# Optimization experiments

Hardware: AMD Instinct MI355X
Metric: run time of the kernel (lower is better)

## Reference

```python
import jax, jax.numpy as jnp
import numpy as np
import math

D = 128
LAMBDA_INIT = 0.8 - 0.6 * math.exp(-0.3 * 1)  # depth=1


def _clin(xr, xi, wr, wi, br, bi):
    # complex linear: (xr + i xi) @ (wr + i wi)^T + (br + i bi)
    o_r = jnp.einsum('bhsd,od->bhso', xr, wr) - jnp.einsum('bhsd,od->bhso', xi, wi) + br
    o_i = jnp.einsum('bhsd,od->bhso', xr, wi) + jnp.einsum('bhsd,od->bhso', xi, wr) + bi
    return o_r, o_i


def setup_inputs() -> dict:
    key = jax.random.key(0)
    ks = jax.random.split(key, 32)
    B, H, S = 1, 12, 1024
    shp = (B, H, S, D)
    inp = {}
    names = ['q_r', 'q_i', 'k_r', 'k_i', 'v_r', 'v_i', 'pe_q_r', 'pe_q_i', 'pe_k_r', 'pe_k_i']
    for i, n in enumerate(names):
        inp[n] = jax.random.normal(ks[i], shp, dtype=jnp.float32)
    std = 1.0 / math.sqrt(D)
    inp['qw_r'] = jax.random.normal(ks[10], (2 * D, D), jnp.float32) * std
    inp['qw_i'] = jax.random.normal(ks[11], (2 * D, D), jnp.float32) * std
    inp['qb_r'] = jnp.zeros((2 * D,), jnp.float32)
    inp['qb_i'] = jnp.zeros((2 * D,), jnp.float32)
    for j, p in enumerate(['k', 'v', 'g', 'o']):
        inp[p + 'w_r'] = jax.random.normal(ks[12 + 2 * j], (D, D), jnp.float32) * std
        inp[p + 'w_i'] = jax.random.normal(ks[13 + 2 * j], (D, D), jnp.float32) * std
        inp[p + 'b_r'] = jnp.zeros((D,), jnp.float32)
        inp[p + 'b_i'] = jnp.zeros((D,), jnp.float32)
    inp['lq1'] = jax.random.normal(ks[20], (D,), jnp.float32) * 0.1
    inp['lk1'] = jax.random.normal(ks[21], (D,), jnp.float32) * 0.1
    inp['lq2'] = jax.random.normal(ks[22], (D,), jnp.float32) * 0.1
    inp['lk2'] = jax.random.normal(ks[23], (D,), jnp.float32) * 0.1
    inp['sub_w'] = jnp.ones((2 * D,), jnp.float32)
    return inp


def _forward(q_r, q_i, k_r, k_i, v_r, v_i, pe_q_r, pe_q_i, pe_k_r, pe_k_i,
             qw_r, qw_i, qb_r, qb_i, kw_r, kw_i, kb_r, kb_i,
             vw_r, vw_i, vb_r, vb_i, gw_r, gw_i, gb_r, gb_i,
             ow_r, ow_i, ob_r, ob_i, lq1, lk1, lq2, lk2, sub_w):
    scale = D ** (-0.5)
    qp_r, qp_i = _clin(q_r, q_i, qw_r, qw_i, qb_r, qb_i)   # [B,H,S,2D]
    kp_r, kp_i = _clin(k_r, k_i, kw_r, kw_i, kb_r, kb_i)   # [B,H,S,D]
    vp_r, vp_i = _clin(v_r, v_i, vw_r, vw_i, vb_r, vb_i)
    qp_r = qp_r + jnp.concatenate([pe_q_r, pe_q_r], axis=-1)
    qp_i = qp_i + jnp.concatenate([pe_q_i, pe_q_i], axis=-1)
    kp_r = kp_r + pe_k_r
    kp_i = kp_i + pe_k_i
    q1_r, q2_r = jnp.split(qp_r, 2, axis=-1)
    q1_i, q2_i = jnp.split(qp_i, 2, axis=-1)

    def attn_w(qr, qi):
        s_r = jnp.einsum('bhqd,bhkd->bhqk', qr, kp_r) + jnp.einsum('bhqd,bhkd->bhqk', qi, kp_i)
        s_i = jnp.einsum('bhqd,bhkd->bhqk', qi, kp_r) - jnp.einsum('bhqd,bhkd->bhqk', qr, kp_i)
        mag = jnp.sqrt(s_r ** 2 + s_i ** 2 + 1e-8) * scale
        return jax.nn.softmax(mag.astype(jnp.float32), axis=-1).astype(s_r.dtype)

    w1 = attn_w(q1_r, q1_i)
    w2 = attn_w(q2_r, q2_i)
    a1_r = jnp.einsum('bhqk,bhkd->bhqd', w1, vp_r)
    a1_i = jnp.einsum('bhqk,bhkd->bhqd', w1, vp_i)
    a2_r = jnp.einsum('bhqk,bhkd->bhqd', w2, vp_r)
    a2_i = jnp.einsum('bhqk,bhkd->bhqd', w2, vp_i)
    cat_r = jnp.concatenate([a1_r, a2_r], axis=-1)
    cat_i = jnp.concatenate([a1_i, a2_i], axis=-1)
    rms = jnp.sqrt(jnp.mean(cat_r ** 2 + cat_i ** 2, axis=-1, keepdims=True) + 1e-5)
    cat_r = cat_r / rms * sub_w
    cat_i = cat_i / rms * sub_w
    a1_r, a2_r = jnp.split(cat_r, 2, axis=-1)
    a1_i, a2_i = jnp.split(cat_i, 2, axis=-1)
    lam1 = jnp.exp(jnp.sum(lq1 * lk1))
    lam2 = jnp.exp(jnp.sum(lq2 * lk2))
    lam = jax.nn.sigmoid(lam1 - lam2 + LAMBDA_INIT)
    out_r = a1_r - lam * a2_r
    out_i = a1_i - lam * a2_i
    g_r, g_i = _clin(q_r, q_i, gw_r, gw_i, gb_r, gb_i)
    out_r, out_i = g_r * out_r - g_i * out_i, g_r * out_i + g_i * out_r
    out_r, out_i = _clin(out_r, out_i, ow_r, ow_i, ob_r, ob_i)
    return out_r, out_i


def reference(q_r, q_i, k_r, k_i, v_r, v_i, pe_q_r, pe_q_i, pe_k_r, pe_k_i,
              qw_r, qw_i, qb_r, qb_i, kw_r, kw_i, kb_r, kb_i,
              vw_r, vw_i, vb_r, vb_i, gw_r, gw_i, gb_r, gb_i,
              ow_r, ow_i, ob_r, ob_i, lq1, lk1, lq2, lk2, sub_w):
    return _forward(q_r, q_i, k_r, k_i, v_r, v_i, pe_q_r, pe_q_i, pe_k_r, pe_k_i,
                    qw_r, qw_i, qb_r, qb_i, kw_r, kw_i, kb_r, kb_i,
                    vw_r, vw_i, vb_r, vb_i, gw_r, gw_i, gb_r, gb_i,
                    ow_r, ow_i, ob_r, ob_i, lq1, lk1, lq2, lk2, sub_w)
```

## Files before the change

kernel.cpp:

```cpp
#include <hip/hip_runtime.h>
#include <math.h>

#define H 12
#define S 1024
#define D 128
#define NROWS (H * S)

typedef __attribute__((ext_vector_type(8))) _Float16 f16x8;
typedef __attribute__((ext_vector_type(4))) float f32x4;
typedef __attribute__((ext_vector_type(4))) int i32x4;

__device__ __forceinline__ short f2h(float f) {
    _Float16 h = (_Float16)f;
    return __builtin_bit_cast(short, h);
}
__device__ __forceinline__ f16x8 fneg8(f16x8 v) {
    i32x4 u = __builtin_bit_cast(i32x4, v);
    u ^= (int)0x80008000;
    return __builtin_bit_cast(f16x8, u);
}

#define WS_QP_R   0ULL
#define WS_QP_I   6291456ULL
#define WS_KP_R   12582912ULL
#define WS_KP_I   15728640ULL
#define WS_VPT_R  18874368ULL
#define WS_VPT_I  22020096ULL
#define WS_G_R    25165824ULL
#define WS_G_I    31457280ULL
#define WS_ACAT_R 37748736ULL
#define WS_ACAT_I 50331648ULL
#define WS_LAM    62914560ULL
#define WS_SC     62914816ULL
#define W16_PER_HEAD  4194304ULL

__global__ void lam_kernel(const float* __restrict__ lq1, const float* __restrict__ lk1,
                           const float* __restrict__ lq2, const float* __restrict__ lk2,
                           float* __restrict__ lam_out)
{
    int t = threadIdx.x;
    float p1 = lq1[t] * lk1[t];
    float p2 = lq2[t] * lk2[t];
    #pragma unroll
    for (int off = 32; off; off >>= 1) {
        p1 += __shfl_xor(p1, off);
        p2 += __shfl_xor(p2, off);
    }
    __shared__ float s1[2], s2[2];
    if ((t & 63) == 0) { s1[t >> 6] = p1; s2[t >> 6] = p2; }
    __syncthreads();
    if (t == 0) {
        float l1 = expf(s1[0] + s1[1]);
        float l2 = expf(s2[0] + s2[1]);
        float x = l1 - l2 + 0.3555090675909693f;
        lam_out[0] = 1.0f / (1.0f + expf(-x));
    }
}

__global__ __launch_bounds__(256) void proj_all(
    const float* __restrict__ q_r, const float* __restrict__ q_i,
    const float* __restrict__ k_r, const float* __restrict__ k_i,
    const float* __restrict__ v_r, const float* __restrict__ v_i,
    const float* __restrict__ pe_q_r, const float* __restrict__ pe_q_i,
    const float* __restrict__ pe_k_r, const float* __restrict__ pe_k_i,
    const float* __restrict__ qw_r, const float* __restrict__ qw_i,
    const float* __restrict__ qb_r, const float* __restrict__ qb_i,
    const float* __restrict__ kw_r, const float* __restrict__ kw_i,
    const float* __restrict__ kb_r, const float* __restrict__ kb_i,
    const float* __restrict__ vw_r, const float* __restrict__ vw_i,
    const float* __restrict__ vb_r, const float* __restrict__ vb_i,
    const float* __restrict__ gw_r, const float* __restrict__ gw_i,
    const float* __restrict__ gb_r, const float* __restrict__ gb_i,
    short* __restrict__ qp_r, short* __restrict__ qp_i,
    short* __restrict__ kp_r, short* __restrict__ kp_i,
    short* __restrict__ vpT_r, short* __restrict__ vpT_i,
    float* __restrict__ g_r, float* __restrict__ g_i)
{
    const int y = blockIdx.y;
    const float *xr, *xi, *wr, *wi, *br, *bi, *per = nullptr, *pei = nullptr;
    void *outr_, *outi_;
    int M, omode, col0;
    if (y < 4)      { xr = q_r; xi = q_i; wr = qw_r; wi = qw_i; br = qb_r; bi = qb_i;
                      per = pe_q_r; pei = pe_q_i; outr_ = qp_r; outi_ = qp_i;
                      M = 256; omode = 1; col0 = y * 64; }
    else if (y < 6) { xr = k_r; xi = k_i; wr = kw_r; wi = kw_i; br = kb_r; bi = kb_i;
                      per = pe_k_r; pei = pe_k_i; outr_ = kp_r; outi_ = kp_i;
                      M = 128; omode = 1; col0 = (y - 4) * 64; }
    else if (y < 8) { xr = v_r; xi = v_i; wr = vw_r; wi = vw_i; br = vb_r; bi = vb_i;
                      outr_ = vpT_r; outi_ = vpT_i;
                      M = 128; omode = 2; col0 = (y - 6) * 64; }
    else            { xr = q_r; xi = q_i; wr = gw_r; wi = gw_i; br = gb_r; bi = gb_i;
                      outr_ = g_r; outi_ = g_i;
                      M = 128; omode = 0; col0 = (y - 8) * 64; }

    __shared__ short As[128 * 72], Brs[64 * 72], Bis[64 * 72];
    const int t = threadIdx.x;
    const int row0 = blockIdx.x * 128;
    const int lane = t & 63, wid = t >> 6;
    const int wm = (wid >> 1) * 64, wn = (wid & 1) * 32;
    const int fm = lane & 15, fq = lane >> 4;
    f32x4 zero4 = {0.f, 0.f, 0.f, 0.f};
    f32x4 accr[4][2], acci[4][2];
    #pragma unroll
    for (int i = 0; i < 4; ++i)
        #pragma unroll
        for (int j = 0; j < 2; ++j) { accr[i][j] = zero4; acci[i][j] = zero4; }

    for (int c = 0; c < 4; ++c) {
        const bool hi = (c >= 2);
        const int kb = (c & 1) * 64;
        const float* Asrc = hi ? xi : xr;
        const float* Brsrc = hi ? wi : wr;
        const float* Bisrc = hi ? wr : wi;
        const float bsign = hi ? -1.0f : 1.0f;
        __syncthreads();
        #pragma unroll
        for (int it = 0; it < 8; ++it) {
            int lin = it * 256 + t;
            int r = lin >> 4, k4 = (lin & 15) * 4;
            float4 va = *(const float4*)&Asrc[(size_t)(row0 + r) * 128 + kb + k4];
            *(short4*)&As[r * 72 + k4] = make_short4(f2h(va.x), f2h(va.y), f2h(va.z), f2h(va.w));
        }
        #pragma unroll
        for (int it = 0; it < 4; ++it) {
            int lin = it * 256 + t;
            int r = lin >> 4, k4 = (lin & 15) * 4;
            float4 vr = *(const float4*)&Brsrc[(size_t)(col0 + r) * 128 + kb + k4];
            *(short4*)&Brs[r * 72 + k4] = make_short4(f2h(bsign * vr.x), f2h(bsign * vr.y),
                                                      f2h(bsign * vr.z), f2h(bsign * vr.w));
            float4 vi = *(const float4*)&Bisrc[(size_t)(col0 + r) * 128 + kb + k4];
            *(short4*)&Bis[r * 72 + k4] = make_short4(f2h(vi.x), f2h(vi.y), f2h(vi.z), f2h(vi.w));
        }
        __syncthreads();
        #pragma unroll
        for (int ks = 0; ks < 64; ks += 32) {
            f16x8 bfr[2], bfi[2];
            #pragma unroll
            for (int j = 0; j < 2; ++j) {
                bfr[j] = *(const f16x8*)&Brs[(wn + j * 16 + fm) * 72 + ks + fq * 8];
                bfi[j] = *(const f16x8*)&Bis[(wn + j * 16 + fm) * 72 + ks + fq * 8];
            }
            #pragma unroll
            for (int i = 0; i < 4; ++i) {
                f16x8 a = *(const f16x8*)&As[(wm + i * 16 + fm) * 72 + ks + fq * 8];
                #pragma unroll
                for (int j = 0; j < 2; ++j) {
                    accr[i][j] = __builtin_amdgcn_mfma_f32_16x16x32_f16(a, bfr[j], accr[i][j], 0, 0, 0);
                    acci[i][j] = __builtin_amdgcn_mfma_f32_16x16x32_f16(a, bfi[j], acci[i][j], 0, 0, 0);
                }
            }
        }
    }
    #pragma unroll
    for (int i = 0; i < 4; ++i)
        #pragma unroll
        for (int j = 0; j < 2; ++j) {
            int colc = col0 + wn + j * 16 + fm;
            float bbr = br[colc], bbi = bi[colc];
            if (omode == 2) {
                int rb = row0 + wm + i * 16 + fq * 4;
                int hq = rb >> 10, sq = rb & 1023;
                short4 o_r4 = make_short4(f2h(accr[i][j][0] + bbr), f2h(accr[i][j][1] + bbr),
                                          f2h(accr[i][j][2] + bbr), f2h(accr[i][j][3] + bbr));
                short4 o_i4 = make_short4(f2h(acci[i][j][0] + bbi), f2h(acci[i][j][1] + bbi),
                                          f2h(acci[i][j][2] + bbi), f2h(acci[i][j][3] + bbi));
                size_t ob = ((size_t)(hq * 128 + colc)) * 1024 + sq;
                *(short4*)&((short*)outr_)[ob] = o_r4;
                *(short4*)&((short*)outi_)[ob] = o_i4;
            } else {
                #pragma unroll
                for (int reg = 0; reg < 4; ++reg) {
                    int rr = row0 + wm + i * 16 + fq * 4 + reg;
                    float o_r = accr[i][j][reg] + bbr;
                    float o_i = acci[i][j][reg] + bbi;
                    if (per) {
                        o_r += per[(size_t)rr * 128 + (colc & 127)];
                        o_i += pei[(size_t)rr * 128 + (colc & 127)];
                    }
                    if (omode == 1) {
                        ((short*)outr_)[(size_t)rr * M + colc] = f2h(o_r);
                        ((short*)outi_)[(size_t)rr * M + colc] = f2h(o_i);
                    } else {
                        ((float*)outr_)[(size_t)rr * M + colc] = o_r;
                        ((float*)outi_)[(size_t)rr * M + colc] = o_i;
                    }
                }
            }
        }
}

__global__ __launch_bounds__(256) void oproj_mfma(
    const float* __restrict__ xr, const float* __restrict__ xi,
    const float* __restrict__ wr, const float* __restrict__ wi,
    const float* __restrict__ br, const float* __restrict__ bi,
    float* __restrict__ outr, float* __restrict__ outi)
{
    __shared__ short As[128 * 72], Brs[64 * 72], Bis[64 * 72];
    const int t = threadIdx.x;
    const int row0 = blockIdx.x * 128, col0 = blockIdx.y * 64;
    const int lane = t & 63, wid = t >> 6;
    const int wm = (wid >> 1) * 64, wn = (wid & 1) * 32;
    const int fm = lane & 15, fq = lane >> 4;
    f32x4 zero4 = {0.f, 0.f, 0.f, 0.f};
    f32x4 accr[4][2], acci[4][2];
    #pragma unroll
    for (int i = 0; i < 4; ++i)
        #pragma unroll
        for (int j = 0; j < 2; ++j) { accr[i][j] = zero4; acci[i][j] = zero4; }

    for (int c = 0; c < 4; ++c) {
        const bool hi = (c >= 2);
        const int kb = (c & 1) * 64;
        const float* Asrc = hi ? xi : xr;
        const float* Brsrc = hi ? wi : wr;
        const float* Bisrc = hi ? wr : wi;
        const float bsign = hi ? -1.0f : 1.0f;
        __syncthreads();
        #pragma unroll
        for (int it = 0; it < 8; ++it) {
            int lin = it * 256 + t;
            int r = lin >> 4, k4 = (lin & 15) * 4;
            float4 va = *(const float4*)&Asrc[(size_t)(row0 + r) * 128 + kb + k4];
            *(short4*)&As[r * 72 + k4] = make_short4(f2h(va.x), f2h(va.y), f2h(va.z), f2h(va.w));
        }
        #pragma unroll
        for (int it = 0; it < 4; ++it) {
            int lin = it * 256 + t;
            int r = lin >> 4, k4 = (lin & 15) * 4;
            float4 vr = *(const float4*)&Brsrc[(size_t)(col0 + r) * 128 + kb + k4];
            *(short4*)&Brs[r * 72 + k4] = make_short4(f2h(bsign * vr.x), f2h(bsign * vr.y),
                                                      f2h(bsign * vr.z), f2h(bsign * vr.w));
            float4 vi = *(const float4*)&Bisrc[(size_t)(col0 + r) * 128 + kb + k4];
            *(short4*)&Bis[r * 72 + k4] = make_short4(f2h(vi.x), f2h(vi.y), f2h(vi.z), f2h(vi.w));
        }
        __syncthreads();
        #pragma unroll
        for (int ks = 0; ks < 64; ks += 32) {
            f16x8 bfr[2], bfi[2];
            #pragma unroll
            for (int j = 0; j < 2; ++j) {
                bfr[j] = *(const f16x8*)&Brs[(wn + j * 16 + fm) * 72 + ks + fq * 8];
                bfi[j] = *(const f16x8*)&Bis[(wn + j * 16 + fm) * 72 + ks + fq * 8];
            }
            #pragma unroll
            for (int i = 0; i < 4; ++i) {
                f16x8 a = *(const f16x8*)&As[(wm + i * 16 + fm) * 72 + ks + fq * 8];
                #pragma unroll
                for (int j = 0; j < 2; ++j) {
                    accr[i][j] = __builtin_amdgcn_mfma_f32_16x16x32_f16(a, bfr[j], accr[i][j], 0, 0, 0);
                    acci[i][j] = __builtin_amdgcn_mfma_f32_16x16x32_f16(a, bfi[j], acci[i][j], 0, 0, 0);
                }
            }
        }
    }
    #pragma unroll
    for (int i = 0; i < 4; ++i)
        #pragma unroll
        for (int j = 0; j < 2; ++j) {
            int colc = col0 + wn + j * 16 + fm;
            float bbr = br[colc], bbi = bi[colc];
            #pragma unroll
            for (int reg = 0; reg < 4; ++reg) {
                int rr = row0 + wm + i * 16 + fq * 4 + reg;
                outr[(size_t)rr * 128 + colc] = accr[i][j][reg] + bbr;
                outi[(size_t)rr * 128 + colc] = acci[i][j][reg] + bbi;
            }
        }
}

__global__ __launch_bounds__(256) void score_mfma(
    const short* __restrict__ qp_r, const short* __restrict__ qp_i,
    const short* __restrict__ kp_r, const short* __restrict__ kp_i,
    short* __restrict__ w16, int h0)
{
    __shared__ short Qr[64 * 72], Qi[64 * 72], Kt[128 * 72];
    const int t = threadIdx.x;
    const int hh = blockIdx.z >> 1, map = blockIdx.z & 1;
    const int h = h0 + hh;
    const int q0 = blockIdx.x * 64, c0 = blockIdx.y * 128;
    const int lane = t & 63, wid = t >> 6;
    const int wm = (wid >> 1) * 32, wn = (wid & 1) * 64;
    const int fm = lane & 15, fq = lane >> 4;
    f32x4 zero4 = {0.f, 0.f, 0.f, 0.f};
    f32x4 sr[2][4], si[2][4];
    #pragma unroll
    for (int i = 0; i < 2; ++i)
        #pragma unroll
        for (int j = 0; j < 4; ++j) { sr[i][j] = zero4; si[i][j] = zero4; }

    for (int kb = 0; kb < 2; ++kb) {
        const int kbase = map * 128 + kb * 64;
        __syncthreads();
        #pragma unroll
        for (int i = 0; i < 4; ++i) {
            int lin = i * 256 + t;
            int r = lin >> 4, k4 = (lin & 15) * 4;
            size_t qb = (size_t)(h * S + q0 + r) * 256 + kbase + k4;
            *(short4*)&Qr[r * 72 + k4] = *(const short4*)&qp_r[qb];
            *(short4*)&Qi[r * 72 + k4] = *(const short4*)&qp_i[qb];
        }
        #pragma unroll
        for (int i = 0; i < 8; ++i) {
            int lin = i * 256 + t;
            int r = lin >> 4, k4 = (lin & 15) * 4;
            *(short4*)&Kt[r * 72 + k4] =
                *(const short4*)&kp_r[(size_t)(h * S + c0 + r) * 128 + kb * 64 + k4];
        }
        __syncthreads();
        f16x8 aR[2][2], aI[2][2];
        #pragma unroll
        for (int ks = 0; ks < 2; ++ks)
            #pragma unroll
            for (int i = 0; i < 2; ++i) {
                int ao = (wm + i * 16 + fm) * 72 + ks * 32 + fq * 8;
                aR[ks][i] = *(const f16x8*)&Qr[ao];
                aI[ks][i] = *(const f16x8*)&Qi[ao];
            }
        #pragma unroll
        for (int ks = 0; ks < 2; ++ks) {
            f16x8 b[4];
            #pragma unroll
            for (int j = 0; j < 4; ++j)
                b[j] = *(const f16x8*)&Kt[(wn + j * 16 + fm) * 72 + ks * 32 + fq * 8];
            #pragma unroll
            for (int i = 0; i < 2; ++i)
                #pragma unroll
                for (int j = 0; j < 4; ++j) {
                    sr[i][j] = __builtin_amdgcn_mfma_f32_16x16x32_f16(aR[ks][i], b[j], sr[i][j], 0, 0, 0);
                    si[i][j] = __builtin_amdgcn_mfma_f32_16x16x32_f16(aI[ks][i], b[j], si[i][j], 0, 0, 0);
                }
        }
        __syncthreads();
        #pragma unroll
        for (int i = 0; i < 8; ++i) {
            int lin = i * 256 + t;
            int r = lin >> 4, k4 = (lin & 15) * 4;
            *(short4*)&Kt[r * 72 + k4] =
                *(const short4*)&kp_i[(size_t)(h * S + c0 + r) * 128 + kb * 64 + k4];
        }
        __syncthreads();
        #pragma unroll
        for (int ks = 0; ks < 2; ++ks) {
            f16x8 b[4];
            #pragma unroll
            for (int j = 0; j < 4; ++j)
                b[j] = *(const f16x8*)&Kt[(wn + j * 16 + fm) * 72 + ks * 32 + fq * 8];
            f16x8 nR0 = fneg8(aR[ks][0]), nR1 = fneg8(aR[ks][1]);
            #pragma unroll
            for (int j = 0; j < 4; ++j) {
                sr[0][j] = __builtin_amdgcn_mfma_f32_16x16x32_f16(aI[ks][0], b[j], sr[0][j], 0, 0, 0);
                si[0][j] = __builtin_amdgcn_mfma_f32_16x16x32_f16(nR0, b[j], si[0][j], 0, 0, 0);
                sr[1][j] = __builtin_amdgcn_mfma_f32_16x16x32_f16(aI[ks][1], b[j], sr[1][j], 0, 0, 0);
                si[1][j] = __builtin_amdgcn_mfma_f32_16x16x32_f16(nR1, b[j], si[1][j], 0, 0, 0);
            }
        }
    }
    const float scale = 0.08838834764831845f;
    #pragma unroll
    for (int i = 0; i < 2; ++i)
        #pragma unroll
        for (int j = 0; j < 4; ++j) {
            int kcol = c0 + wn + j * 16 + fm;
            #pragma unroll
            for (int reg = 0; reg < 4; ++reg) {
                int q = q0 + wm + i * 16 + fq * 4 + reg;
                float r1 = sr[i][j][reg], I1 = si[i][j][reg];
                float m1 = sqrtf(fmaf(r1, r1, fmaf(I1, I1, 1e-8f))) * scale;
                w16[(((size_t)hh * 2 + map) * S + q) * S + kcol] = f2h(m1);
            }
        }
}

__global__ __launch_bounds__(256) void softmax_f16(short* __restrict__ w16)
{
    short* row = w16 + (size_t)blockIdx.x * S;
    int t = threadIdx.x;
    short4 s = ((short4*)row)[t];
    float f0 = (float)__builtin_bit_cast(_Float16, s.x);
    float f1 = (float)__builtin_bit_cast(_Float16, s.y);
    float f2v = (float)__builtin_bit_cast(_Float16, s.z);
    float f3 = (float)__builtin_bit_cast(_Float16, s.w);
    float m = fmaxf(fmaxf(f0, f1), fmaxf(f2v, f3));
    #pragma unroll
    for (int off = 32; off; off >>= 1) m = fmaxf(m, __shfl_xor(m, off));
    __shared__ float redm[4], reds[4];
    int w = t >> 6;
    if ((t & 63) == 0) redm[w] = m;
    __syncthreads();
    m = fmaxf(fmaxf(redm[0], redm[1]), fmaxf(redm[2], redm[3]));
    float e0 = __expf(f0 - m), e1 = __expf(f1 - m), e2 = __expf(f2v - m), e3 = __expf(f3 - m);
    float ssum = e0 + e1 + e2 + e3;
    #pragma unroll
    for (int off = 32; off; off >>= 1) ssum += __shfl_xor(ssum, off);
    if ((t & 63) == 0) reds[w] = ssum;
    __syncthreads();
    ssum = reds[0] + reds[1] + reds[2] + reds[3];
    float inv = 1.0f / ssum;
    s.x = f2h(e0 * inv); s.y = f2h(e1 * inv); s.z = f2h(e2 * inv); s.w = f2h(e3 * inv);
    ((short4*)row)[t] = s;
}

__global__ __launch_bounds__(256) void av_mfma(
    const short* __restrict__ w16, const short* __restrict__ vpT_r, const short* __restrict__ vpT_i,
    float* __restrict__ acat_r, float* __restrict__ acat_i, int h0)
{
    __shared__ short W1[64 * 72], W2[64 * 72], Vc[128 * 72];
    const int t = threadIdx.x;
    const int hh = blockIdx.z, h = h0 + hh;
    const int comp = blockIdx.y;
    const int q0 = blockIdx.x * 64;
    const short* vpT = comp ? vpT_i : vpT_r;
    float* acat = comp ? acat_i : acat_r;
    const int lane = t & 63, wid = t >> 6;
    const int wm = (wid >> 1) * 32, wn = (wid & 1) * 64;
    const int fm = lane & 15, fq = lane >> 4;
    f32x4 zero4 = {0.f, 0.f, 0.f, 0.f};
    f32x4 a1[2][4], a2[2][4];
    #pragma unroll
    for (int i = 0; i < 2; ++i)
        #pragma unroll
        for (int j = 0; j < 4; ++j) { a1[i][j] = zero4; a2[i][j] = zero4; }

    for (int k0 = 0; k0 < S; k0 += 64) {
        __syncthreads();
        #pragma unroll
        for (int it = 0; it < 4; ++it) {
            int lin = it * 256 + t;
            int r = lin >> 4, k4 = (lin & 15) * 4;
            *(short4*)&W1[r * 72 + k4] = *(const short4*)&w16[(((size_t)hh * 2 + 0) * S + q0 + r) * S + k0 + k4];
            *(short4*)&W2[r * 72 + k4] = *(const short4*)&w16[(((size_t)hh * 2 + 1) * S + q0 + r) * S + k0 + k4];
        }
        #pragma unroll
        for (int it = 0; it < 8; ++it) {
            int lin = it * 256 + t;
            int dd = lin >> 4, k4 = (lin & 15) * 4;
            *(short4*)&Vc[dd * 72 + k4] = *(const short4*)&vpT[(size_t)(h * 128 + dd) * 1024 + k0 + k4];
        }
        __syncthreads();
        #pragma unroll
        for (int ks = 0; ks < 64; ks += 32) {
            f16x8 b[4];
            #pragma unroll
            for (int j = 0; j < 4; ++j)
                b[j] = *(const f16x8*)&Vc[(wn + j * 16 + fm) * 72 + ks + fq * 8];
            #pragma unroll
            for (int i = 0; i < 2; ++i) {
                int wo = (wm + i * 16 + fm) * 72 + ks + fq * 8;
                f16x8 w1f = *(const f16x8*)&W1[wo];
                f16x8 w2f = *(const f16x8*)&W2[wo];
                #pragma unroll
                for (int j = 0; j < 4; ++j) {
                    a1[i][j] = __builtin_amdgcn_mfma_f32_16x16x32_f16(w1f, b[j], a1[i][j], 0, 0, 0);
                    a2[i][j] = __builtin_amdgcn_mfma_f32_16x16x32_f16(w2f, b[j], a2[i][j], 0, 0, 0);
                }
            }
        }
    }
    #pragma unroll
    for (int i = 0; i < 2; ++i)
        #pragma unroll
        for (int j = 0; j < 4; ++j) {
            int d = wn + j * 16 + fm;
            #pragma unroll
            for (int reg = 0; reg < 4; ++reg) {
                int q = q0 + wm + i * 16 + fq * 4 + reg;
                size_t rowb = (size_t)(h * S + q) * 256;
                acat[rowb + d]       = a1[i][j][reg];
                acat[rowb + 128 + d] = a2[i][j][reg];
            }
        }
}

__global__ __launch_bounds__(256) void rmsgate_kernel(
    const float* __restrict__ acat_r, const float* __restrict__ acat_i,
    const float* __restrict__ sub_w, const float* __restrict__ lam_ptr,
    float* __restrict__ g_r, float* __restrict__ g_i)
{
    int row = blockIdx.x;
    int t = threadIdx.x;
    float ar = acat_r[(size_t)row * 256 + t];
    float ai = acat_i[(size_t)row * 256 + t];
    float ss = fmaf(ar, ar, ai * ai);
    #pragma unroll
    for (int off = 32; off; off >>= 1) ss += __shfl_xor(ss, off);
    __shared__ float red[4];
    if ((t & 63) == 0) red[t >> 6] = ss;
    __syncthreads();
    float total = red[0] + red[1] + red[2] + red[3];
    float inv_rms = 1.0f / sqrtf(total * (1.0f / 256.0f) + 1e-5f);
    float sw = sub_w[t];
    __shared__ float Cr[256], Ci[256];
    Cr[t] = ar * inv_rms * sw;
    Ci[t] = ai * inv_rms * sw;
    __syncthreads();
    if (t < 128) {
        float lam = lam_ptr[0];
        float o_r = Cr[t] - lam * Cr[t + 128];
        float o_i = Ci[t] - lam * Ci[t + 128];
        float gr = g_r[(size_t)row * 128 + t];
        float gi = g_i[(size_t)row * 128 + t];
        g_r[(size_t)row * 128 + t] = gr * o_r - gi * o_i;
        g_i[(size_t)row * 128 + t] = gr * o_i + gi * o_r;
    }
}

extern "C" void kernel_launch(void* const* d_in, const int* in_sizes, int n_in,
                              void* d_out, int out_size, void* d_ws, size_t ws_size,
                              hipStream_t stream)
{
    (void)in_sizes; (void)n_in; (void)out_size;
    const float* q_r    = (const float*)d_in[0];
    const float* q_i    = (const float*)d_in[1];
    const float* k_r    = (const float*)d_in[2];
    const float* k_i    = (const float*)d_in[3];
    const float* v_r    = (const float*)d_in[4];
    const float* v_i    = (const float*)d_in[5];
    const float* pe_q_r = (const float*)d_in[6];
    const float* pe_q_i = (const float*)d_in[7];
    const float* pe_k_r = (const float*)d_in[8];
    const float* pe_k_i = (const float*)d_in[9];
    const float* qw_r   = (const float*)d_in[10];
    const float* qw_i   = (const float*)d_in[11];
    const float* qb_r   = (const float*)d_in[12];
    const float* qb_i   = (const float*)d_in[13];
    const float* kw_r   = (const float*)d_in[14];
    const float* kw_i   = (const float*)d_in[15];
    const float* kb_r   = (const float*)d_in[16];
    const float* kb_i   = (const float*)d_in[17];
    const float* vw_r   = (const float*)d_in[18];
    const float* vw_i   = (const float*)d_in[19];
    const float* vb_r   = (const float*)d_in[20];
    const float* vb_i   = (const float*)d_in[21];
    const float* gw_r   = (const float*)d_in[22];
    const float* gw_i   = (const float*)d_in[23];
    const float* gb_r   = (const float*)d_in[24];
    const float* gb_i   = (const float*)d_in[25];
    const float* ow_r   = (const float*)d_in[26];
    const float* ow_i   = (const float*)d_in[27];
    const float* ob_r   = (const float*)d_in[28];
    const float* ob_i   = (const float*)d_in[29];
    const float* lq1    = (const float*)d_in[30];
    const float* lk1    = (const float*)d_in[31];
    const float* lq2    = (const float*)d_in[32];
    const float* lk2    = (const float*)d_in[33];
    const float* sub_w  = (const float*)d_in[34];

    char* ws = (char*)d_ws;
    short* qp_r   = (short*)(ws + WS_QP_R);
    short* qp_i   = (short*)(ws + WS_QP_I);
    short* kp_r   = (short*)(ws + WS_KP_R);
    short* kp_i   = (short*)(ws + WS_KP_I);
    short* vpT_r  = (short*)(ws + WS_VPT_R);
    short* vpT_i  = (short*)(ws + WS_VPT_I);
    float* g_r    = (float*)(ws + WS_G_R);
    float* g_i    = (float*)(ws + WS_G_I);
    float* acat_r = (float*)(ws + WS_ACAT_R);
    float* acat_i = (float*)(ws + WS_ACAT_I);
    float* lam    = (float*)(ws + WS_LAM);
    short* w16    = (short*)(ws + WS_SC);

    float* out_r = (float*)d_out;
    float* out_i = out_r + (size_t)NROWS * D;

    size_t avail = ws_size > WS_SC ? ws_size - WS_SC : 0;
    int nh_chunk = (int)(avail / W16_PER_HEAD);
    if (nh_chunk < 1) nh_chunk = 1;
    if (nh_chunk > H) nh_chunk = H;

    lam_kernel<<<1, 128, 0, stream>>>(lq1, lk1, lq2, lk2, lam);

    proj_all<<<dim3(96, 10), 256, 0, stream>>>(
        q_r, q_i, k_r, k_i, v_r, v_i, pe_q_r, pe_q_i, pe_k_r, pe_k_i,
        qw_r, qw_i, qb_r, qb_i, kw_r, kw_i, kb_r, kb_i,
        vw_r, vw_i, vb_r, vb_i, gw_r, gw_i, gb_r, gb_i,
        qp_r, qp_i, kp_r, kp_i, vpT_r, vpT_i, g_r, g_i);

    for (int h0 = 0; h0 < H; h0 += nh_chunk) {
        int nhh = (H - h0 < nh_chunk) ? (H - h0) : nh_chunk;
        score_mfma<<<dim3(16, 8, nhh * 2), 256, 0, stream>>>(qp_r, qp_i, kp_r, kp_i, w16, h0);
        softmax_f16<<<nhh * 2 * S, 256, 0, stream>>>(w16);
        av_mfma<<<dim3(16, 2, nhh), 256, 0, stream>>>(w16, vpT_r, vpT_i, acat_r, acat_i, h0);
    }

    rmsgate_kernel<<<NROWS, 256, 0, stream>>>(acat_r, acat_i, sub_w, lam, g_r, g_i);

    oproj_mfma<<<dim3(96, 2), 256, 0, stream>>>(g_r, g_i, ow_r, ow_i, ob_r, ob_i, out_r, out_i);
}
```

Measured before the change: 318.3 us.

## Fold softmax normalization into AV loads, shrink tiles, store intermediates in fp16

The softmax kernel now only computes per-row max and inverse sum, and no longer rewrites the score matrix. The AV kernel applies exp and normalization while loading scores into shared memory, which removes one full read-modify-write pass over the fp16 score buffer. The gate, attention-concat and gated intermediates are stored as fp16 instead of fp32 to halve their traffic. Row tiles in proj, oproj and av are halved, doubling the block count for better occupancy. The cost is that each AV block recomputes exp for its score tile, and the fp16 intermediates lose some precision.

New measurement: 294.4 us. -7.5%, faster.

```diff
diff --git a/kernel.cpp b/kernel.cpp
--- a/kernel.cpp
+++ b/kernel.cpp
@@ -13,6 +13,9 @@
 __device__ __forceinline__ short f2h(float f) {
     _Float16 h = (_Float16)f;
     return __builtin_bit_cast(short, h);
+}
+__device__ __forceinline__ float h2f(short s) {
+    return (float)__builtin_bit_cast(_Float16, s);
 }
 __device__ __forceinline__ f16x8 fneg8(f16x8 v) {
     i32x4 u = __builtin_bit_cast(i32x4, v);
@@ -26,13 +29,14 @@
 #define WS_KP_I   15728640ULL
 #define WS_VPT_R  18874368ULL
 #define WS_VPT_I  22020096ULL
-#define WS_G_R    25165824ULL
-#define WS_G_I    31457280ULL
-#define WS_ACAT_R 37748736ULL
-#define WS_ACAT_I 50331648ULL
-#define WS_LAM    62914560ULL
-#define WS_SC     62914816ULL
-#define W16_PER_HEAD  4194304ULL
+#define WS_GP_R   25165824ULL
+#define WS_GP_I   28311552ULL
+#define WS_ACAT_R 31457280ULL
+#define WS_ACAT_I 37748736ULL
+#define WS_LAM    44040192ULL
+#define WS_SC     44040448ULL
+#define W16_PER_HEAD   4194304ULL
+#define STAT_PER_HEAD  16384ULL
 
 __global__ void lam_kernel(const float* __restrict__ lq1, const float* __restrict__ lk1,
                            const float* __restrict__ lq2, const float* __restrict__ lk2,
@@ -74,11 +78,11 @@
     short* __restrict__ qp_r, short* __restrict__ qp_i,
     short* __restrict__ kp_r, short* __restrict__ kp_i,
     short* __restrict__ vpT_r, short* __restrict__ vpT_i,
-    float* __restrict__ g_r, float* __restrict__ g_i)
+    short* __restrict__ gp_r, short* __restrict__ gp_i)
 {
     const int y = blockIdx.y;
     const float *xr, *xi, *wr, *wi, *br, *bi, *per = nullptr, *pei = nullptr;
-    void *outr_, *outi_;
+    short *outr_, *outi_;
     int M, omode, col0;
     if (y < 4)      { xr = q_r; xi = q_i; wr = qw_r; wi = qw_i; br = qb_r; bi = qb_i;
                       per = pe_q_r; pei = pe_q_i; outr_ = qp_r; outi_ = qp_i;
@@ -90,19 +94,19 @@
                       outr_ = vpT_r; outi_ = vpT_i;
                       M = 128; omode = 2; col0 = (y - 6) * 64; }
     else            { xr = q_r; xi = q_i; wr = gw_r; wi = gw_i; br = gb_r; bi = gb_i;
-                      outr_ = g_r; outi_ = g_i;
-                      M = 128; omode = 0; col0 = (y - 8) * 64; }
-
-    __shared__ short As[128 * 72], Brs[64 * 72], Bis[64 * 72];
+                      outr_ = gp_r; outi_ = gp_i;
+                      M = 128; omode = 1; col0 = (y - 8) * 64; }
+
+    __shared__ short As[64 * 72], Brs[64 * 72], Bis[64 * 72];
     const int t = threadIdx.x;
-    const int row0 = blockIdx.x * 128;
+    const int row0 = blockIdx.x * 64;
     const int lane = t & 63, wid = t >> 6;
-    const int wm = (wid >> 1) * 64, wn = (wid & 1) * 32;
+    const int wm = (wid >> 1) * 32, wn = (wid & 1) * 32;
     const int fm = lane & 15, fq = lane >> 4;
     f32x4 zero4 = {0.f, 0.f, 0.f, 0.f};
-    f32x4 accr[4][2], acci[4][2];
-    #pragma unroll
-    for (int i = 0; i < 4; ++i)
+    f32x4 accr[2][2], acci[2][2];
+    #pragma unroll
+    for (int i = 0; i < 2; ++i)
         #pragma unroll
         for (int j = 0; j < 2; ++j) { accr[i][j] = zero4; acci[i][j] = zero4; }
 
@@ -115,16 +119,11 @@
         const float bsign = hi ? -1.0f : 1.0f;
         __syncthreads();
         #pragma unroll
-        for (int it = 0; it < 8; ++it) {
+        for (int it = 0; it < 4; ++it) {
             int lin = it * 256 + t;
             int r = lin >> 4, k4 = (lin & 15) * 4;
             float4 va = *(const float4*)&Asrc[(size_t)(row0 + r) * 128 + kb + k4];
             *(short4*)&As[r * 72 + k4] = make_short4(f2h(va.x), f2h(va.y), f2h(va.z), f2h(va.w));
-        }
-        #pragma unroll
-        for (int it = 0; it < 4; ++it) {
-            int lin = it * 256 + t;
-            int r = lin >> 4, k4 = (lin & 15) * 4;
             float4 vr = *(const float4*)&Brsrc[(size_t)(col0 + r) * 128 + kb + k4];
             *(short4*)&Brs[r * 72 + k4] = make_short4(f2h(bsign * vr.x), f2h(bsign * vr.y),
                                                       f2h(bsign * vr.z), f2h(bsign * vr.w));
@@ -141,7 +140,7 @@
                 bfi[j] = *(const f16x8*)&Bis[(wn + j * 16 + fm) * 72 + ks + fq * 8];
             }
             #pragma unroll
-            for (int i = 0; i < 4; ++i) {
+            for (int i = 0; i < 2; ++i) {
                 f16x8 a = *(const f16x8*)&As[(wm + i * 16 + fm) * 72 + ks + fq * 8];
                 #pragma unroll
                 for (int j = 0; j < 2; ++j) {
@@ -152,7 +151,7 @@
         }
     }
     #pragma unroll
-    for (int i = 0; i < 4; ++i)
+    for (int i = 0; i < 2; ++i)
         #pragma unroll
         for (int j = 0; j < 2; ++j) {
             int colc = col0 + wn + j * 16 + fm;
@@ -165,8 +164,8 @@
                 short4 o_i4 = make_short4(f2h(acci[i][j][0] + bbi), f2h(acci[i][j][1] + bbi),
                                           f2h(acci[i][j][2] + bbi), f2h(acci[i][j][3] + bbi));
                 size_t ob = ((size_t)(hq * 128 + colc)) * 1024 + sq;
-                *(short4*)&((short*)outr_)[ob] = o_r4;
-                *(short4*)&((short*)outi_)[ob] = o_i4;
+                *(short4*)&outr_[ob] = o_r4;
+                *(short4*)&outi_[ob] = o_i4;
             } else {
                 #pragma unroll
                 for (int reg = 0; reg < 4; ++reg) {
@@ -177,56 +176,45 @@
                         o_r += per[(size_t)rr * 128 + (colc & 127)];
                         o_i += pei[(size_t)rr * 128 + (colc & 127)];
                     }
-                    if (omode == 1) {
-                        ((short*)outr_)[(size_t)rr * M + colc] = f2h(o_r);
-                        ((short*)outi_)[(size_t)rr * M + colc] = f2h(o_i);
-                    } else {
-                        ((float*)outr_)[(size_t)rr * M + colc] = o_r;
-                        ((float*)outi_)[(size_t)rr * M + colc] = o_i;
-                    }
+                    outr_[(size_t)rr * M + colc] = f2h(o_r);
+                    outi_[(size_t)rr * M + colc] = f2h(o_i);
                 }
             }
         }
 }
 
 __global__ __launch_bounds__(256) void oproj_mfma(
-    const float* __restrict__ xr, const float* __restrict__ xi,
+    const short* __restrict__ gp_r, const short* __restrict__ gp_i,
     const float* __restrict__ wr, const float* __restrict__ wi,
     const float* __restrict__ br, const float* __restrict__ bi,
     float* __restrict__ outr, float* __restrict__ outi)
 {
-    __shared__ short As[128 * 72], Brs[64 * 72], Bis[64 * 72];
+    __shared__ short As[64 * 72], Brs[64 * 72], Bis[64 * 72];
     const int t = threadIdx.x;
-    const int row0 = blockIdx.x * 128, col0 = blockIdx.y * 64;
+    const int row0 = blockIdx.x * 64, col0 = blockIdx.y * 64;
     const int lane = t & 63, wid = t >> 6;
-    const int wm = (wid >> 1) * 64, wn = (wid & 1) * 32;
+    const int wm = (wid >> 1) * 32, wn = (wid & 1) * 32;
     const int fm = lane & 15, fq = lane >> 4;
     f32x4 zero4 = {0.f, 0.f, 0.f, 0.f};
-    f32x4 accr[4][2], acci[4][2];
-    #pragma unroll
-    for (int i = 0; i < 4; ++i)
+    f32x4 accr[2][2], acci[2][2];
+    #pragma unroll
+    for (int i = 0; i < 2; ++i)
         #pragma unroll
         for (int j = 0; j < 2; ++j) { accr[i][j] = zero4; acci[i][j] = zero4; }
 
     for (int c = 0; c < 4; ++c) {
         const bool hi = (c >= 2);
         const int kb = (c & 1) * 64;
-        const float* Asrc = hi ? xi : xr;
+        const short* Asrc = hi ? gp_i : gp_r;
         const float* Brsrc = hi ? wi : wr;
         const float* Bisrc = hi ? wr : wi;
         const float bsign = hi ? -1.0f : 1.0f;
         __syncthreads();
         #pragma unroll
-        for (int it = 0; it < 8; ++it) {
-            int lin = it * 256 + t;
-            int r = lin >> 4, k4 = (lin & 15) * 4;
-            float4 va = *(const float4*)&Asrc[(size_t)(row0 + r) * 128 + kb + k4];
-            *(short4*)&As[r * 72 + k4] = make_short4(f2h(va.x), f2h(va.y), f2h(va.z), f2h(va.w));
-        }
-        #pragma unroll
         for (int it = 0; it < 4; ++it) {
             int lin = it * 256 + t;
             int r = lin >> 4, k4 = (lin & 15) * 4;
+            *(short4*)&As[r * 72 + k4] = *(const short4*)&Asrc[(size_t)(row0 + r) * 128 + kb + k4];
             float4 vr = *(const float4*)&Brsrc[(size_t)(col0 + r) * 128 + kb + k4];
             *(short4*)&Brs[r * 72 + k4] = make_short4(f2h(bsign * vr.x), f2h(bsign * vr.y),
                                                       f2h(bsign * vr.z), f2h(bsign * vr.w));
@@ -243,7 +231,7 @@
                 bfi[j] = *(const f16x8*)&Bis[(wn + j * 16 + fm) * 72 + ks + fq * 8];
             }
             #pragma unroll
-            for (int i = 0; i < 4; ++i) {
+            for (int i = 0; i < 2; ++i) {
                 f16x8 a = *(const f16x8*)&As[(wm + i * 16 + fm) * 72 + ks + fq * 8];
                 #pragma unroll
                 for (int j = 0; j < 2; ++j) {
@@ -254,7 +242,7 @@
         }
     }
     #pragma unroll
-    for (int i = 0; i < 4; ++i)
+    for (int i = 0; i < 2; ++i)
         #pragma unroll
         for (int j = 0; j < 2; ++j) {
             int colc = col0 + wn + j * 16 + fm;
@@ -371,15 +359,13 @@
         }
 }
 
-__global__ __launch_bounds__(256) void softmax_f16(short* __restrict__ w16)
-{
-    short* row = w16 + (size_t)blockIdx.x * S;
+__global__ __launch_bounds__(256) void smstats(const short* __restrict__ w16,
+                                               float2* __restrict__ stats)
+{
+    const short* row = w16 + (size_t)blockIdx.x * S;
     int t = threadIdx.x;
-    short4 s = ((short4*)row)[t];
-    float f0 = (float)__builtin_bit_cast(_Float16, s.x);
-    float f1 = (float)__builtin_bit_cast(_Float16, s.y);
-    float f2v = (float)__builtin_bit_cast(_Float16, s.z);
-    float f3 = (float)__builtin_bit_cast(_Float16, s.w);
+    short4 s = ((const short4*)row)[t];
+    float f0 = h2f(s.x), f1 = h2f(s.y), f2v = h2f(s.z), f3 = h2f(s.w);
     float m = fmaxf(fmaxf(f0, f1), fmaxf(f2v, f3));
     #pragma unroll
     for (int off = 32; off; off >>= 1) m = fmaxf(m, __shfl_xor(m, off));
@@ -388,47 +374,55 @@
     if ((t & 63) == 0) redm[w] = m;
     __syncthreads();
     m = fmaxf(fmaxf(redm[0], redm[1]), fmaxf(redm[2], redm[3]));
-    float e0 = __expf(f0 - m), e1 = __expf(f1 - m), e2 = __expf(f2v - m), e3 = __expf(f3 - m);
-    float ssum = e0 + e1 + e2 + e3;
+    float ssum = __expf(f0 - m) + __expf(f1 - m) + __expf(f2v - m) + __expf(f3 - m);
     #pragma unroll
     for (int off = 32; off; off >>= 1) ssum += __shfl_xor(ssum, off);
     if ((t & 63) == 0) reds[w] = ssum;
     __syncthreads();
-    ssum = reds[0] + reds[1] + reds[2] + reds[3];
-    float inv = 1.0f / ssum;
-    s.x = f2h(e0 * inv); s.y = f2h(e1 * inv); s.z = f2h(e2 * inv); s.w = f2h(e3 * inv);
-    ((short4*)row)[t] = s;
+    if (t == 0) {
+        float total = reds[0] + reds[1] + reds[2] + reds[3];
+        stats[blockIdx.x] = make_float2(m, 1.0f / total);
+    }
 }
 
 __global__ __launch_bounds__(256) void av_mfma(
-    const short* __restrict__ w16, const short* __restrict__ vpT_r, const short* __restrict__ vpT_i,
-    float* __restrict__ acat_r, float* __restrict__ acat_i, int h0)
-{
-    __shared__ short W1[64 * 72], W2[64 * 72], Vc[128 * 72];
+    const short* __restrict__ w16, const float2* __restrict__ stats,
+    const short* __restrict__ vpT_r, const short* __restrict__ vpT_i,
+    short* __restrict__ acat_r, short* __restrict__ acat_i, int h0)
+{
+    __shared__ short W1[32 * 72], W2[32 * 72], Vc[128 * 72];
     const int t = threadIdx.x;
     const int hh = blockIdx.z, h = h0 + hh;
     const int comp = blockIdx.y;
-    const int q0 = blockIdx.x * 64;
+    const int q0 = blockIdx.x * 32;
     const short* vpT = comp ? vpT_i : vpT_r;
-    float* acat = comp ? acat_i : acat_r;
+    short* acat = comp ? acat_i : acat_r;
+    const float2* st1 = stats + ((size_t)hh * 2 + 0) * S;
+    const float2* st2 = stats + ((size_t)hh * 2 + 1) * S;
     const int lane = t & 63, wid = t >> 6;
-    const int wm = (wid >> 1) * 32, wn = (wid & 1) * 64;
+    const int wm = (wid >> 1) * 16, wn = (wid & 1) * 64;
     const int fm = lane & 15, fq = lane >> 4;
     f32x4 zero4 = {0.f, 0.f, 0.f, 0.f};
-    f32x4 a1[2][4], a2[2][4];
-    #pragma unroll
-    for (int i = 0; i < 2; ++i)
-        #pragma unroll
-        for (int j = 0; j < 4; ++j) { a1[i][j] = zero4; a2[i][j] = zero4; }
+    f32x4 a1[4], a2[4];
+    #pragma unroll
+    for (int j = 0; j < 4; ++j) { a1[j] = zero4; a2[j] = zero4; }
 
     for (int k0 = 0; k0 < S; k0 += 64) {
         __syncthreads();
         #pragma unroll
-        for (int it = 0; it < 4; ++it) {
+        for (int it = 0; it < 2; ++it) {
             int lin = it * 256 + t;
             int r = lin >> 4, k4 = (lin & 15) * 4;
-            *(short4*)&W1[r * 72 + k4] = *(const short4*)&w16[(((size_t)hh * 2 + 0) * S + q0 + r) * S + k0 + k4];
-            *(short4*)&W2[r * 72 + k4] = *(const short4*)&w16[(((size_t)hh * 2 + 1) * S + q0 + r) * S + k0 + k4];
+            float2 s1v = st1[q0 + r];
+            float2 s2v = st2[q0 + r];
+            short4 m1 = *(const short4*)&w16[(((size_t)hh * 2 + 0) * S + q0 + r) * S + k0 + k4];
+            short4 m2 = *(const short4*)&w16[(((size_t)hh * 2 + 1) * S + q0 + r) * S + k0 + k4];
+            *(short4*)&W1[r * 72 + k4] = make_short4(
+                f2h(__expf(h2f(m1.x) - s1v.x) * s1v.y), f2h(__expf(h2f(m1.y) - s1v.x) * s1v.y),
+                f2h(__expf(h2f(m1.z) - s1v.x) * s1v.y), f2h(__expf(h2f(m1.w) - s1v.x) * s1v.y));
+            *(short4*)&W2[r * 72 + k4] = make_short4(
+                f2h(__expf(h2f(m2.x) - s2v.x) * s2v.y), f2h(__expf(h2f(m2.y) - s2v.x) * s2v.y),
+                f2h(__expf(h2f(m2.z) - s2v.x) * s2v.y), f2h(__expf(h2f(m2.w) - s2v.x) * s2v.y));
         }
         #pragma unroll
         for (int it = 0; it < 8; ++it) {
@@ -443,43 +437,38 @@
             #pragma unroll
             for (int j = 0; j < 4; ++j)
                 b[j] = *(const f16x8*)&Vc[(wn + j * 16 + fm) * 72 + ks + fq * 8];
-            #pragma unroll
-            for (int i = 0; i < 2; ++i) {
-                int wo = (wm + i * 16 + fm) * 72 + ks + fq * 8;
-                f16x8 w1f = *(const f16x8*)&W1[wo];
-                f16x8 w2f = *(const f16x8*)&W2[wo];
-                #pragma unroll
-                for (int j = 0; j < 4; ++j) {
-                    a1[i][j] = __builtin_amdgcn_mfma_f32_16x16x32_f16(w1f, b[j], a1[i][j], 0, 0, 0);
-                    a2[i][j] = __builtin_amdgcn_mfma_f32_16x16x32_f16(w2f, b[j], a2[i][j], 0, 0, 0);
-                }
-            }
-        }
-    }
-    #pragma unroll
-    for (int i = 0; i < 2; ++i)
-        #pragma unroll
-        for (int j = 0; j < 4; ++j) {
-            int d = wn + j * 16 + fm;
-            #pragma unroll
-            for (int reg = 0; reg < 4; ++reg) {
-                int q = q0 + wm + i * 16 + fq * 4 + reg;
-                size_t rowb = (size_t)(h * S + q) * 256;
-                acat[rowb + d]       = a1[i][j][reg];
-                acat[rowb + 128 + d] = a2[i][j][reg];
-            }
-        }
+            int wo = (wm + fm) * 72 + ks + fq * 8;
+            f16x8 w1f = *(const f16x8*)&W1[wo];
+            f16x8 w2f = *(const f16x8*)&W2[wo];
+            #pragma unroll
+            for (int j = 0; j < 4; ++j) {
+                a1[j] = __builtin_amdgcn_mfma_f32_16x16x32_f16(w1f, b[j], a1[j], 0, 0, 0);
+                a2[j] = __builtin_amdgcn_mfma_f32_16x16x32_f16(w2f, b[j], a2[j], 0, 0, 0);
+            }
+        }
+    }
+    #pragma unroll
+    for (int j = 0; j < 4; ++j) {
+        int d = wn + j * 16 + fm;
+        #pragma unroll
+        for (int reg = 0; reg < 4; ++reg) {
+            int q = q0 + wm + fq * 4 + reg;
+            size_t rowb = (size_t)(h * S + q) * 256;
+            acat[rowb + d]       = f2h(a1[j][reg]);
+            acat[rowb + 128 + d] = f2h(a2[j][reg]);
+        }
+    }
 }
 
 __global__ __launch_bounds__(256) void rmsgate_kernel(
-    const float* __restrict__ acat_r, const float* __restrict__ acat_i,
+    const short* __restrict__ acat_r, const short* __restrict__ acat_i,
     const float* __restrict__ sub_w, const float* __restrict__ lam_ptr,
-    float* __restrict__ g_r, float* __restrict__ g_i)
+    short* __restrict__ gp_r, short* __restrict__ gp_i)
 {
     int row = blockIdx.x;
     int t = threadIdx.x;
-    float ar = acat_r[(size_t)row * 256 + t];
-    float ai = acat_i[(size_t)row * 256 + t];
+    float ar = h2f(acat_r[(size_t)row * 256 + t]);
+    float ai = h2f(acat_i[(size_t)row * 256 + t]);
     float ss = fmaf(ar, ar, ai * ai);
     #pragma unroll
     for (int off = 32; off; off >>= 1) ss += __shfl_xor(ss, off);
@@ -497,10 +486,10 @@
         float lam = lam_ptr[0];
         float o_r = Cr[t] - lam * Cr[t + 128];
         float o_i = Ci[t] - lam * Ci[t + 128];
-        float gr = g_r[(size_t)row * 128 + t];
-        float gi = g_i[(size_t)row * 128 + t];
-        g_r[(size_t)row * 128 + t] = gr * o_r - gi * o_i;
-        g_i[(size_t)row * 128 + t] = gr * o_i + gi * o_r;
+        float gr = h2f(gp_r[(size_t)row * 128 + t]);
+        float gi = h2f(gp_i[(size_t)row * 128 + t]);
+        gp_r[(size_t)row * 128 + t] = f2h(gr * o_r - gi * o_i);
+        gp_i[(size_t)row * 128 + t] = f2h(gr * o_i + gi * o_r);
     }
 }
 
@@ -552,10 +541,10 @@
     short* kp_i   = (short*)(ws + WS_KP_I);
     short* vpT_r  = (short*)(ws + WS_VPT_R);
     short* vpT_i  = (short*)(ws + WS_VPT_I);
-    float* g_r    = (float*)(ws + WS_G_R);
-    float* g_i    = (float*)(ws + WS_G_I);
-    float* acat_r = (float*)(ws + WS_ACAT_R);
-    float* acat_i = (float*)(ws + WS_ACAT_I);
+    short* gp_r   = (short*)(ws + WS_GP_R);
+    short* gp_i   = (short*)(ws + WS_GP_I);
+    short* acat_r = (short*)(ws + WS_ACAT_R);
+    short* acat_i = (short*)(ws + WS_ACAT_I);
     float* lam    = (float*)(ws + WS_LAM);
     short* w16    = (short*)(ws + WS_SC);
 
@@ -563,26 +552,27 @@
     float* out_i = out_r + (size_t)NROWS * D;
 
     size_t avail = ws_size > WS_SC ? ws_size - WS_SC : 0;
-    int nh_chunk = (int)(avail / W16_PER_HEAD);
+    int nh_chunk = (int)(avail / (W16_PER_HEAD + STAT_PER_HEAD));
     if (nh_chunk < 1) nh_chunk = 1;
     if (nh_chunk > H) nh_chunk = H;
+    float2* stats = (float2*)(ws + WS_SC + (size_t)nh_chunk * W16_PER_HEAD);
 
     lam_kernel<<<1, 128, 0, stream>>>(lq1, lk1, lq2, lk2, lam);
 
-    proj_all<<<dim3(96, 10), 256, 0, stream>>>(
+    proj_all<<<dim3(192, 10), 256, 0, stream>>>(
         q_r, q_i, k_r, k_i, v_r, v_i, pe_q_r, pe_q_i, pe_k_r, pe_k_i,
         qw_r, qw_i, qb_r, qb_i, kw_r, kw_i, kb_r, kb_i,
         vw_r, vw_i, vb_r, vb_i, gw_r, gw_i, gb_r, gb_i,
-        qp_r, qp_i, kp_r, kp_i, vpT_r, vpT_i, g_r, g_i);
+        qp_r, qp_i, kp_r, kp_i, vpT_r, vpT_i, gp_r, gp_i);
 
     for (int h0 = 0; h0 < H; h0 += nh_chunk) {
         int nhh = (H - h0 < nh_chunk) ? (H - h0) : nh_chunk;
         score_mfma<<<dim3(16, 8, nhh * 2), 256, 0, stream>>>(qp_r, qp_i, kp_r, kp_i, w16, h0);
-        softmax_f16<<<nhh * 2 * S, 256, 0, stream>>>(w16);
-        av_mfma<<<dim3(16, 2, nhh), 256, 0, stream>>>(w16, vpT_r, vpT_i, acat_r, acat_i, h0);
-    }
-
-    rmsgate_kernel<<<NROWS, 256, 0, stream>>>(acat_r, acat_i, sub_w, lam, g_r, g_i);
-
-    oproj_mfma<<<dim3(96, 2), 256, 0, stream>>>(g_r, g_i, ow_r, ow_i, ob_r, ob_i, out_r, out_i);
-}
+        smstats<<<nhh * 2 * S, 256, 0, stream>>>(w16, stats);
+        av_mfma<<<dim3(32, 2, nhh), 256, 0, stream>>>(w16, stats, vpT_r, vpT_i, acat_r, acat_i, h0);
+    }
+
+    rmsgate_kernel<<<NROWS, 256, 0, stream>>>(acat_r, acat_i, sub_w, lam, gp_r, gp_i);
+
+    oproj_mfma<<<dim3(192, 2), 256, 0, stream>>>(gp_r, gp_i, ow_r, ow_i, ob_r, ob_i, out_r, out_i);
+}
```
